# Performance work log

Measured on AMD Instinct MI355X. Metric: run time of the kernel, lower is better.

The kernel has to match this reference:

```python
import jax, jax.numpy as jnp
import numpy as np

N_NODES = 100000
N_EDGES = 1000000
F_IN = 64
F_HID = 32


def setup_inputs() -> dict:
    key = jax.random.key(0)
    k = jax.random.split(key, 6)
    x = jax.random.normal(k[0], (N_NODES, F_IN), dtype=jnp.float32)
    edge_index = jax.random.randint(k[1], (2, N_EDGES), 0, N_NODES, dtype=jnp.int32)
    # Glorot-ish scaled weights (PyG GCNConv linear has no bias; bias added post-aggregation)
    W1 = jax.random.normal(k[2], (F_IN, F_HID), dtype=jnp.float32) / np.sqrt(F_IN)
    b1 = jax.random.normal(k[3], (F_HID,), dtype=jnp.float32) * 0.01
    W2 = jax.random.normal(k[4], (F_HID, F_IN), dtype=jnp.float32) / np.sqrt(F_HID)
    b2 = jax.random.normal(k[5], (F_IN,), dtype=jnp.float32) * 0.01
    return {"x": x, "edge_index": edge_index, "W1": W1, "b1": b1, "W2": W2, "b2": b2}


def gcn_conv(x, W, b, src, dst, n):
    """PyG GCNConv: h = x @ W; add self-loops; symmetric norm; scatter-add; + bias."""
    h = x @ W  # [N, out]
    ones = jnp.ones(src.shape[0], dtype=h.dtype)
    # degree includes the implicit self-loop (+1 per node)
    deg = jax.ops.segment_sum(ones, dst, num_segments=n) + 1.0  # [N]
    dis = jax.lax.rsqrt(deg)  # deg^{-1/2}
    norm = dis[src] * dis[dst]  # [E]
    agg = jax.ops.segment_sum(h[src] * norm[:, None], dst, num_segments=n)
    # self-loop contribution: norm_ii = deg_i^{-1}
    agg = agg + h * (dis * dis)[:, None]
    return agg + b


def reference(x, edge_index, W1, b1, W2, b2):
    src, dst = edge_index[0], edge_index[1]
    n = x.shape[0]
    h = jax.nn.relu(gcn_conv(x, W1, b1, src, dst, n))
    # dropout is identity in eval mode
    return gcn_conv(h, W2, b2, src, dst, n)
```

## Files before the change

kernel.cpp:

```cpp
#include <hip/hip_runtime.h>
#include <hip/hip_fp16.h>

#define NN 100000
#define NE 1000000
#define FIN 64
#define FHID 32
#define NB 782
#define BNODES 128
#define NCH 256
#define CH ((NE + NCH - 1) / NCH)
#define GEMB ((NN + 31) / 32)

union H8 { __half2 h2[4]; float4 f4; };
union H4 { __half2 h2[2]; float2 f2; };

__global__ __launch_bounds__(256) void k_bhist(const int* __restrict__ dst, int* __restrict__ phist) {
    __shared__ int lh[NB];
    for (int i = threadIdx.x; i < NB; i += 256) lh[i] = 0;
    __syncthreads();
    int k = blockIdx.x;
    int e0 = k * CH, e1 = min(e0 + CH, NE);
    for (int e = e0 + threadIdx.x; e < e1; e += 256) atomicAdd(&lh[dst[e] >> 7], 1);
    __syncthreads();
    for (int b = threadIdx.x; b < NB; b += 256) phist[(size_t)k * NB + b] = lh[b];
}

__global__ __launch_bounds__(256) void k_bscan(int* __restrict__ phist, int* __restrict__ btot) {
    int b = blockIdx.x;
    int k = threadIdx.x;
    int v = phist[(size_t)k * NB + b];
    int lane = k & 63, wv = k >> 6;
    int incl = v;
#pragma unroll
    for (int s = 1; s < 64; s <<= 1) {
        int t = __shfl_up(incl, s, 64);
        if (lane >= s) incl += t;
    }
    __shared__ int wt[4];
    if (lane == 63) wt[wv] = incl;
    __syncthreads();
    int add = 0;
#pragma unroll
    for (int w = 0; w < 4; ++w) add += (w < wv) ? wt[w] : 0;
    phist[(size_t)k * NB + b] = add + incl - v;
    if (k == 255) btot[b] = add + incl;
}

__global__ __launch_bounds__(1024) void k_bbase(const int* __restrict__ btot, int* __restrict__ bbase,
                                                int* __restrict__ off) {
    __shared__ int s[1024];
    int b = threadIdx.x;
    int v = (b < NB) ? btot[b] : 0;
    s[b] = v;
    __syncthreads();
    for (int d = 1; d < 1024; d <<= 1) {
        int t = (b >= d) ? s[b - d] : 0;
        __syncthreads();
        s[b] += t;
        __syncthreads();
    }
    if (b < NB) bbase[b] = s[b] - v;
    if (b == 0) { bbase[NB] = NE; off[NN] = NE; }
}

__global__ __launch_bounds__(256) void k_scatter_gemm1(const int* __restrict__ ei,
                                                       const int* __restrict__ phist,
                                                       const int* __restrict__ bbase,
                                                       int* __restrict__ ebuf,
                                                       const float* __restrict__ x,
                                                       const float* __restrict__ W1,
                                                       __half* __restrict__ h1) {
    int r = blockIdx.x;
    bool issc;
    int id;
    if (r < 2 * NCH) { issc = !(r & 1); id = r >> 1; }
    else             { issc = false;    id = r - NCH; }
    if (issc) {
        __shared__ int lh[NB];
        __shared__ int lbase[NB];
        int k = id;
        for (int b = threadIdx.x; b < NB; b += 256) {
            lh[b] = 0;
            lbase[b] = bbase[b] + phist[(size_t)k * NB + b];
        }
        __syncthreads();
        int e0 = k * CH, e1 = min(e0 + CH, NE);
        for (int e = e0 + threadIdx.x; e < e1; e += 256) {
            int s = ei[e], d = ei[NE + e];
            int bb = d >> 7;
            int rr = atomicAdd(&lh[bb], 1);
            ebuf[lbase[bb] + rr] = s * BNODES + (d & 127);
        }
        return;
    }
    __shared__ float Wl[FIN * FHID];
    for (int t = threadIdx.x; t < FIN * FHID / 4; t += 256)
        reinterpret_cast<float4*>(Wl)[t] = reinterpret_cast<const float4*>(W1)[t];
    __syncthreads();
    int row = id * 32 + (threadIdx.x >> 3);
    int l = threadIdx.x & 7;
    if (row >= NN) return;
    const float4* xr = reinterpret_cast<const float4*>(x + (size_t)row * FIN);
    float4 acc = make_float4(0.f, 0.f, 0.f, 0.f);
#pragma unroll
    for (int k4 = 0; k4 < FIN / 4; ++k4) {
        float4 a4 = xr[k4];
#pragma unroll
        for (int j = 0; j < 4; ++j) {
            float a = j == 0 ? a4.x : j == 1 ? a4.y : j == 2 ? a4.z : a4.w;
            const float4 wv = *reinterpret_cast<const float4*>(Wl + (k4 * 4 + j) * FHID + l * 4);
            acc.x += a * wv.x; acc.y += a * wv.y; acc.z += a * wv.z; acc.w += a * wv.w;
        }
    }
    H4 u;
    u.h2[0] = __floats2half2_rn(acc.x, acc.y);
    u.h2[1] = __floats2half2_rn(acc.z, acc.w);
    *reinterpret_cast<float2*>(h1 + (size_t)row * FHID + l * 4) = u.f2;
}

__global__ __launch_bounds__(256) void k_csr(const int* __restrict__ ebuf, const int* __restrict__ bbase,
                                             int* __restrict__ off, float* __restrict__ dis,
                                             int* __restrict__ csr, __half* __restrict__ h1) {
    __shared__ int nh[BNODES];
    __shared__ int ofl[BNODES];
    __shared__ float sdis[BNODES];
    int b = blockIdx.x;
    int n0 = b * BNODES;
    int ebeg = bbase[b], eend = bbase[b + 1];
    int ld = threadIdx.x;
    if (ld < BNODES) nh[ld] = 0;
    __syncthreads();
    for (int e = ebeg + threadIdx.x; e < eend; e += 256) atomicAdd(&nh[ebuf[e] & 127], 1);
    __syncthreads();
    int dval = (ld < BNODES) ? nh[ld] : 0;
    if (ld < BNODES) ofl[ld] = dval;
    __syncthreads();
    for (int s = 1; s < BNODES; s <<= 1) {
        int t = 0;
        if (ld < BNODES && ld >= s) t = ofl[ld - s];
        __syncthreads();
        if (ld < BNODES) ofl[ld] += t;
        __syncthreads();
    }
    if (ld < BNODES) {
        ofl[ld] -= dval;
        float dv = rsqrtf((float)dval + 1.0f);
        sdis[ld] = dv;
        int n = n0 + ld;
        if (n < NN) {
            off[n] = ebeg + ofl[ld];
            dis[n] = dv;
        }
        nh[ld] = 0;
    }
    __syncthreads();
    for (int e = ebeg + threadIdx.x; e < eend; e += 256) {
        int v = ebuf[e];
        int ldd = v & 127;
        int r = atomicAdd(&nh[ldd], 1);
        csr[ebeg + ofl[ldd] + r] = v >> 7;
    }
    int i = ld >> 1, part = ld & 1;
    int n = n0 + i;
    if (n < NN) {
        float dv = sdis[i];
        float4* pr = reinterpret_cast<float4*>(h1 + (size_t)n * FHID + part * 16);
#pragma unroll
        for (int j = 0; j < 2; ++j) {
            float4 v4 = pr[j];
            __half2* hp = reinterpret_cast<__half2*>(&v4);
#pragma unroll
            for (int u = 0; u < 4; ++u) {
                float2 f = __half22float2(hp[u]);
                hp[u] = __floats2half2_rn(f.x * dv, f.y * dv);
            }
            pr[j] = v4;
        }
    }
}

__global__ __launch_bounds__(256) void k_gather1(const int* __restrict__ off, const int* __restrict__ csr,
                                                 const float* __restrict__ dis,
                                                 const __half* __restrict__ h, const float* __restrict__ bias,
                                                 __half* __restrict__ out) {
    int t = blockIdx.x * 256 + threadIdx.x;
    int n = t >> 5;
    int l = t & 31;
    int q = l >> 2, c = l & 3;
    float dn = dis[n];
    int beg = off[n], end = off[n + 1];
    float acc[8] = {0.f, 0.f, 0.f, 0.f, 0.f, 0.f, 0.f, 0.f};
    for (int p = beg + q; p < end; p += 8) {
        int s = csr[p];
        float4 v = *reinterpret_cast<const float4*>(h + (size_t)s * FHID + c * 8);
        const __half2* hp = reinterpret_cast<const __half2*>(&v);
#pragma unroll
        for (int j = 0; j < 4; ++j) {
            float2 f = __half22float2(hp[j]);
            acc[2 * j] += f.x;
            acc[2 * j + 1] += f.y;
        }
    }
#pragma unroll
    for (int j = 0; j < 8; ++j) {
        acc[j] += __shfl_xor(acc[j], 4);
        acc[j] += __shfl_xor(acc[j], 8);
        acc[j] += __shfl_xor(acc[j], 16);
    }
    if (q == 0) {
        float4 sv = *reinterpret_cast<const float4*>(h + (size_t)n * FHID + c * 8);
        const __half2* sp = reinterpret_cast<const __half2*>(&sv);
#pragma unroll
        for (int j = 0; j < 4; ++j) {
            float2 f = __half22float2(sp[j]);
            acc[2 * j] += f.x;
            acc[2 * j + 1] += f.y;
        }
        const float4 b0 = *reinterpret_cast<const float4*>(bias + c * 8);
        const float4 b1v = *reinterpret_cast<const float4*>(bias + c * 8 + 4);
        float bb[8] = {b0.x, b0.y, b0.z, b0.w, b1v.x, b1v.y, b1v.z, b1v.w};
        H8 o;
#pragma unroll
        for (int j = 0; j < 4; ++j) {
            float v0 = dn * acc[2 * j] + bb[2 * j];
            float v1 = dn * acc[2 * j + 1] + bb[2 * j + 1];
            v0 = v0 > 0.f ? v0 : 0.f;
            v1 = v1 > 0.f ? v1 : 0.f;
            o.h2[j] = __floats2half2_rn(dn * v0, dn * v1);
        }
        *reinterpret_cast<float4*>(out + (size_t)n * FHID + c * 8) = o.f4;
    }
}

__global__ __launch_bounds__(256) void k_gather_mm(const int* __restrict__ off, const int* __restrict__ csr,
                                                   const float* __restrict__ dis,
                                                   const __half* __restrict__ h, const float* __restrict__ W2,
                                                   const float* __restrict__ b2, float* __restrict__ out) {
    __shared__ float WL[FHID * FIN];
    __shared__ float aggL[8 * 36];
    for (int t = threadIdx.x; t < FHID * FIN / 4; t += 256)
        reinterpret_cast<float4*>(WL)[t] = reinterpret_cast<const float4*>(W2)[t];

    int i = threadIdx.x >> 5;
    int l = threadIdx.x & 31;
    int q = l >> 2, c = l & 3;
    int n = blockIdx.x * 8 + i;
    {
        float dn = dis[n];
        int beg = off[n], end = off[n + 1];
        float acc[8] = {0.f, 0.f, 0.f, 0.f, 0.f, 0.f, 0.f, 0.f};
        for (int p = beg + q; p < end; p += 8) {
            int s = csr[p];
            float4 v = *reinterpret_cast<const float4*>(h + (size_t)s * FHID + c * 8);
            const __half2* hp = reinterpret_cast<const __half2*>(&v);
#pragma unroll
            for (int j = 0; j < 4; ++j) {
                float2 f = __half22float2(hp[j]);
                acc[2 * j] += f.x;
                acc[2 * j + 1] += f.y;
            }
        }
#pragma unroll
        for (int j = 0; j < 8; ++j) {
            acc[j] += __shfl_xor(acc[j], 4);
            acc[j] += __shfl_xor(acc[j], 8);
            acc[j] += __shfl_xor(acc[j], 16);
        }
        if (q == 0) {
            float4 sv = *reinterpret_cast<const float4*>(h + (size_t)n * FHID + c * 8);
            const __half2* sp = reinterpret_cast<const __half2*>(&sv);
            float* ar = aggL + i * 36 + c * 8;
#pragma unroll
            for (int j = 0; j < 4; ++j) {
                float2 f = __half22float2(sp[j]);
                ar[2 * j] = dn * (acc[2 * j] + f.x);
                ar[2 * j + 1] = dn * (acc[2 * j + 1] + f.y);
            }
        }
    }
    __syncthreads();

    int r = threadIdx.x >> 5;
    int n2 = blockIdx.x * 8 + r;
    int cc = (threadIdx.x & 31) * 2;
    float ax = b2[cc], ay = b2[cc + 1];
    const float* ag = aggL + r * 36;
#pragma unroll
    for (int k = 0; k < FHID; ++k) {
        float a = ag[k];
        ax += a * WL[k * FIN + cc];
        ay += a * WL[k * FIN + cc + 1];
    }
    float2 o2 = make_float2(ax, ay);
    *reinterpret_cast<float2*>(out + (size_t)n2 * FIN + cc) = o2;
}

extern "C" void kernel_launch(void* const* d_in, const int* in_sizes, int n_in,
                              void* d_out, int out_size, void* d_ws, size_t ws_size,
                              hipStream_t stream) {
    const float* x  = (const float*)d_in[0];
    const int*   ei = (const int*)d_in[1];
    const float* W1 = (const float*)d_in[2];
    const float* b1 = (const float*)d_in[3];
    const float* W2 = (const float*)d_in[4];
    const float* b2 = (const float*)d_in[5];
    float* out = (float*)d_out;

    char* w = (char*)d_ws;
    auto align = [](size_t v) { return (v + 255) & ~(size_t)255; };
    int*    phist = (int*)w;    w += align((size_t)NCH * NB * 4);
    int*    btot  = (int*)w;    w += align((size_t)NB * 4);
    int*    bbase = (int*)w;    w += align((size_t)(NB + 1) * 4);
    int*    ebuf  = (int*)w;    w += align((size_t)NE * 4);
    int*    off   = (int*)w;    w += align((size_t)(NN + 1) * 4);
    float*  dis   = (float*)w;  w += align((size_t)NN * 4);
    int*    csr   = (int*)w;    w += align((size_t)NE * 4);
    __half* h1    = (__half*)w; w += align((size_t)NN * FHID * 2);
    __half* hbuf  = (__half*)w; w += align((size_t)NN * FHID * 2);

    const int* dst = ei + NE;
    k_bhist<<<NCH, 256, 0, stream>>>(dst, phist);
    k_bscan<<<NB, 256, 0, stream>>>(phist, btot);
    k_bbase<<<1, 1024, 0, stream>>>(btot, bbase, off);
    k_scatter_gemm1<<<NCH + GEMB, 256, 0, stream>>>(ei, phist, bbase, ebuf, x, W1, h1);
    k_csr<<<NB, 256, 0, stream>>>(ebuf, bbase, off, dis, csr, h1);
    k_gather1<<<(NN * 32) / 256, 256, 0, stream>>>(off, csr, dis, h1, b1, hbuf);
    k_gather_mm<<<NN / 8, 256, 0, stream>>>(off, csr, dis, hbuf, W2, b2, out);
}
```

Before: 111.9 us.

## Use 16 lanes per node in gathers with prefetched CSR indices

Both gather kernels now assign 16 threads to each node instead of 32, so four edges are processed in parallel per iteration, and each block covers 16 nodes. The next CSR index is loaded one iteration ahead so the dependent load of the feature row can overlap with it, and one shuffle reduction step is dropped. The fused matmul epilogue now computes four output columns per thread and writes them with float4 stores and LDS reads. The aim is less idle lane work on average-degree-10 nodes and fewer instructions per edge, at the cost of fewer memory requests in flight per node.

Measured after the change: 95.51 us. -14.6%, faster.

```diff
diff --git a/kernel.cpp b/kernel.cpp
--- a/kernel.cpp
+++ b/kernel.cpp
@@ -184,15 +184,18 @@
                                                  const __half* __restrict__ h, const float* __restrict__ bias,
                                                  __half* __restrict__ out) {
     int t = blockIdx.x * 256 + threadIdx.x;
-    int n = t >> 5;
-    int l = t & 31;
+    int n = t >> 4;
+    int l = t & 15;
     int q = l >> 2, c = l & 3;
     float dn = dis[n];
     int beg = off[n], end = off[n + 1];
     float acc[8] = {0.f, 0.f, 0.f, 0.f, 0.f, 0.f, 0.f, 0.f};
-    for (int p = beg + q; p < end; p += 8) {
-        int s = csr[p];
-        float4 v = *reinterpret_cast<const float4*>(h + (size_t)s * FHID + c * 8);
+    int p = beg + q;
+    int s = (p < end) ? csr[p] : 0;
+    for (; p < end; p += 4) {
+        int scur = s;
+        if (p + 4 < end) s = csr[p + 4];
+        float4 v = *reinterpret_cast<const float4*>(h + (size_t)scur * FHID + c * 8);
         const __half2* hp = reinterpret_cast<const __half2*>(&v);
 #pragma unroll
         for (int j = 0; j < 4; ++j) {
@@ -205,7 +208,6 @@
     for (int j = 0; j < 8; ++j) {
         acc[j] += __shfl_xor(acc[j], 4);
         acc[j] += __shfl_xor(acc[j], 8);
-        acc[j] += __shfl_xor(acc[j], 16);
     }
     if (q == 0) {
         float4 sv = *reinterpret_cast<const float4*>(h + (size_t)n * FHID + c * 8);
@@ -237,21 +239,24 @@
                                                    const __half* __restrict__ h, const float* __restrict__ W2,
                                                    const float* __restrict__ b2, float* __restrict__ out) {
     __shared__ float WL[FHID * FIN];
-    __shared__ float aggL[8 * 36];
+    __shared__ float aggL[16 * 36];
     for (int t = threadIdx.x; t < FHID * FIN / 4; t += 256)
         reinterpret_cast<float4*>(WL)[t] = reinterpret_cast<const float4*>(W2)[t];
 
-    int i = threadIdx.x >> 5;
-    int l = threadIdx.x & 31;
+    int i = threadIdx.x >> 4;
+    int l = threadIdx.x & 15;
     int q = l >> 2, c = l & 3;
-    int n = blockIdx.x * 8 + i;
+    int n = blockIdx.x * 16 + i;
     {
         float dn = dis[n];
         int beg = off[n], end = off[n + 1];
         float acc[8] = {0.f, 0.f, 0.f, 0.f, 0.f, 0.f, 0.f, 0.f};
-        for (int p = beg + q; p < end; p += 8) {
-            int s = csr[p];
-            float4 v = *reinterpret_cast<const float4*>(h + (size_t)s * FHID + c * 8);
+        int p = beg + q;
+        int s = (p < end) ? csr[p] : 0;
+        for (; p < end; p += 4) {
+            int scur = s;
+            if (p + 4 < end) s = csr[p + 4];
+            float4 v = *reinterpret_cast<const float4*>(h + (size_t)scur * FHID + c * 8);
             const __half2* hp = reinterpret_cast<const __half2*>(&v);
 #pragma unroll
             for (int j = 0; j < 4; ++j) {
@@ -264,7 +269,6 @@
         for (int j = 0; j < 8; ++j) {
             acc[j] += __shfl_xor(acc[j], 4);
             acc[j] += __shfl_xor(acc[j], 8);
-            acc[j] += __shfl_xor(acc[j], 16);
         }
         if (q == 0) {
             float4 sv = *reinterpret_cast<const float4*>(h + (size_t)n * FHID + c * 8);
@@ -280,19 +284,18 @@
     }
     __syncthreads();
 
-    int r = threadIdx.x >> 5;
-    int n2 = blockIdx.x * 8 + r;
-    int cc = (threadIdx.x & 31) * 2;
-    float ax = b2[cc], ay = b2[cc + 1];
+    int r = threadIdx.x >> 4;
+    int n2 = blockIdx.x * 16 + r;
+    int c0 = (threadIdx.x & 15) * 4;
+    float4 a0 = *reinterpret_cast<const float4*>(b2 + c0);
     const float* ag = aggL + r * 36;
 #pragma unroll
     for (int k = 0; k < FHID; ++k) {
         float a = ag[k];
-        ax += a * WL[k * FIN + cc];
-        ay += a * WL[k * FIN + cc + 1];
-    }
-    float2 o2 = make_float2(ax, ay);
-    *reinterpret_cast<float2*>(out + (size_t)n2 * FIN + cc) = o2;
+        const float4 wv = *reinterpret_cast<const float4*>(WL + k * FIN + c0);
+        a0.x += a * wv.x; a0.y += a * wv.y; a0.z += a * wv.z; a0.w += a * wv.w;
+    }
+    *reinterpret_cast<float4*>(out + (size_t)n2 * FIN + c0) = a0;
 }
 
 extern "C" void kernel_launch(void* const* d_in, const int* in_sizes, int n_in,
@@ -324,6 +327,6 @@
     k_bbase<<<1, 1024, 0, stream>>>(btot, bbase, off);
     k_scatter_gemm1<<<NCH + GEMB, 256, 0, stream>>>(ei, phist, bbase, ebuf, x, W1, h1);
     k_csr<<<NB, 256, 0, stream>>>(ebuf, bbase, off, dis, csr, h1);
-    k_gather1<<<(NN * 32) / 256, 256, 0, stream>>>(off, csr, dis, h1, b1, hbuf);
-    k_gather_mm<<<NN / 8, 256, 0, stream>>>(off, csr, dis, hbuf, W2, b2, out);
-}
+    k_gather1<<<(NN * 16) / 256, 256, 0, stream>>>(off, csr, dis, h1, b1, hbuf);
+    k_gather_mm<<<NN / 16, 256, 0, stream>>>(off, csr, dis, hbuf, W2, b2, out);
+}
```
